# Optimization experiments

Measured on AMD Instinct MI355X. Metric: run time of the kernel, lower is better.

## Reference

```python
import jax, jax.numpy as jnp
import numpy as np

H, W = 4096, 4096

# Fixed tiny kernels expressed as shifted-slice sums (exactly equivalent to
# F.conv2d with stride=1, padding=0 for these 0/1 kernels).

def _diag(x):   # [[1,0],[0,1]] -> (H-1, W-1)
    return x[:-1, :-1] + x[1:, 1:]

def _anti(x):   # [[0,1],[1,0]]
    return x[:-1, 1:] + x[1:, :-1]

def _all2(x):   # 2x2 all-ones
    return x[:-1, :-1] + x[:-1, 1:] + x[1:, :-1] + x[1:, 1:]

def _cross(x):  # 3x3 plus-shape -> (H-2, W-2)
    return x[:-2, 1:-1] + x[2:, 1:-1] + x[1:-1, :-2] + x[1:-1, 2:]

def setup_inputs() -> dict:
    key = jax.random.key(0)
    board = jax.random.randint(key, (H, W), 0, 3, dtype=jnp.int32)
    return {"board_np": board}

def reference(board_np):
    black = (board_np == 1).astype(jnp.float32)
    white = (board_np == 2).astype(jnp.float32)
    empty = (board_np == 0).astype(jnp.float32)

    black_diag, black_anti = _diag(black), _anti(black)
    white_diag, white_anti = _diag(white), _anti(white)
    empty_diag, empty_anti = _diag(empty), _anti(empty)

    bamboo_black = ((black_diag == 2) & (empty_anti == 2)) | ((black_anti == 2) & (empty_diag == 2))
    bamboo_white = ((white_diag == 2) & (empty_anti == 2)) | ((white_anti == 2) & (empty_diag == 2))

    black_s2, white_s2, empty_s2 = _all2(black), _all2(white), _all2(empty)
    # tmp_de/ae/be/ce: single-cell picks of the 2x2 window
    empty_d = empty[1:, 1:]
    empty_a = empty[:-1, :-1]
    empty_b = empty[:-1, 1:]
    empty_c = empty[1:, :-1]
    any_empty_corner = (empty_d == 1) | (empty_a == 1) | (empty_b == 1) | (empty_c == 1)

    tiger_black = (black_s2 >= 2) & any_empty_corner
    tiger_white = (white_s2 >= 2) & any_empty_corner
    empty_triangle_black = (black_s2 == 3) & (empty_s2 == 1)
    empty_triangle_white = (white_s2 == 3) & (empty_s2 == 1)

    empty_center = empty[1:-1, 1:-1]  # k_center conv
    eye_black = (empty_center == 1) & (_cross(black) == 4)
    eye_white = (empty_center == 1) & (_cross(white) == 4)

    return (bamboo_black, bamboo_white, tiger_black, tiger_white,
            empty_triangle_black, empty_triangle_white, eye_black, eye_white)
```

## Files before the change

kernel.cpp:

```cpp
#include <hip/hip_runtime.h>


#define BW 4096
#define W1 4095
#define W2 4094
#define N1 16769025
#define N2 16760836

typedef int i4a __attribute__((vector_size(16), aligned(16)));

template<int IM4>
__device__ __forceinline__ void store_planes(
    int* __restrict__ out, const int i, const int u, const bool has2,
    const int (&cellm)[7], const int (&eyem)[6])
{
    const bool fullv = (u < 1023);
    const size_t orow = (size_t)i * W1 + (u << 2);

    #pragma unroll
    for (int p = 0; p < 6; ++p) {
        const int sp = (IM4 - p) & 3;
        int* dst = out + (size_t)p * N1 + orow;
        if (fullv) {
            i4a s;
            s[0] = (cellm[sp + 0] >> p) & 1;
            s[1] = (cellm[sp + 1] >> p) & 1;
            s[2] = (cellm[sp + 2] >> p) & 1;
            s[3] = (cellm[sp + 3] >> p) & 1;
            *(i4a*)(dst + sp) = s;
        } else {
            #pragma unroll
            for (int k = 0; k < 3 - sp; ++k)
                dst[sp + k] = (cellm[sp + k] >> p) & 1;
        }
        if (u == 0) {
            #pragma unroll
            for (int k = 0; k < sp; ++k)
                dst[k] = (cellm[k] >> p) & 1;
        }
    }

    if (has2) {
        const int e = (IM4 & 1) ? 0 : 2;
        int* d0 = out + (size_t)6 * N1 + (size_t)i * W2 + (u << 2);
        int* d1 = d0 + N2;
        if (fullv) {
            i4a s0, s1;
            #pragma unroll
            for (int k = 0; k < 4; ++k) {
                s0[k] =  eyem[e + k]       & 1;
                s1[k] = (eyem[e + k] >> 1) & 1;
            }
            *(i4a*)(d0 + e) = s0;
            *(i4a*)(d1 + e) = s1;
        } else if (e == 0) {
            #pragma unroll
            for (int k = 0; k < 2; ++k) {
                d0[k] =  eyem[k]       & 1;
                d1[k] = (eyem[k] >> 1) & 1;
            }
        }
        if (u == 0) {
            #pragma unroll
            for (int k = 0; k < e; ++k) {
                d0[k] =  eyem[k]       & 1;
                d1[k] = (eyem[k] >> 1) & 1;
            }
        }
    }
}

__global__ __launch_bounds__(256)
void motif_kernel(const int* __restrict__ board, int* __restrict__ out) {
    const int u = blockIdx.x * 256 + threadIdx.x;
    const int i = blockIdx.y;
    const int base = u << 2;
    const bool fullv = (u < 1023);
    const bool has2  = (i < W2);

    const int* p0 = board + (size_t)i * BW + base;
    const int* p1 = p0 + BW;
    const int* p2 = p1 + BW;

    i4a a0 = *(const i4a*)p0;
    i4a a1 = *(const i4a*)p1;
    i4a b0 = {0, 0, 0, 0}, b1 = {0, 0, 0, 0};
    if (fullv) { b0 = *(const i4a*)(p0 + 4); b1 = *(const i4a*)(p1 + 4); }
    i4a a2 = {0, 0, 0, 0}, b2 = {0, 0, 0, 0};
    if (has2) {
        a2 = *(const i4a*)p2;
        if (fullv) b2 = *(const i4a*)(p2 + 4);
    }

    const int r0[8] = {a0[0], a0[1], a0[2], a0[3], b0[0], b0[1], b0[2], b0[3]};
    const int r1[8] = {a1[0], a1[1], a1[2], a1[3], b1[0], b1[1], b1[2], b1[3]};
    const int r2[8] = {a2[0], a2[1], a2[2], a2[3], b2[0], b2[1], b2[2], b2[3]};

    int cellm[7];
    #pragma unroll
    for (int p = 0; p < 7; ++p) {
        const int a = r0[p], b = r0[p + 1], c = r1[p], d = r1[p + 1];
        const int nb_d = (a == 1) + (d == 1), nb_a = (b == 1) + (c == 1);
        const int nw_d = (a == 2) + (d == 2), nw_a = (b == 2) + (c == 2);
        const int ne_d = (a == 0) + (d == 0), ne_a = (b == 0) + (c == 0);
        const int nb = nb_d + nb_a, nw = nw_d + nw_a, ne = ne_d + ne_a;
        const int bb  = ((nb_d == 2) & (ne_a == 2)) | ((nb_a == 2) & (ne_d == 2));
        const int bw_ = ((nw_d == 2) & (ne_a == 2)) | ((nw_a == 2) & (ne_d == 2));
        const int anyE = (ne >= 1);
        const int tb = (nb >= 2) & anyE;
        const int tw = (nw >= 2) & anyE;
        const int eb = (nb == 3) & (ne == 1);
        const int ew = (nw == 3) & (ne == 1);
        cellm[p] = bb | (bw_ << 1) | (tb << 2) | (tw << 3) | (eb << 4) | (ew << 5);
    }

    int eyem[6];
    #pragma unroll
    for (int q = 0; q < 6; ++q) {
        const int ce = r1[q + 1], up = r0[q + 1], lf = r1[q],
                  dn = r2[q + 1], rt = r1[q + 2];
        const int eB = (ce == 0) & (up == 1) & (lf == 1) & (dn == 1) & (rt == 1);
        const int eW = (ce == 0) & (up == 2) & (lf == 2) & (dn == 2) & (rt == 2);
        eyem[q] = eB | (eW << 1);
    }

    switch (i & 3) {
        case 0: store_planes<0>(out, i, u, has2, cellm, eyem); break;
        case 1: store_planes<1>(out, i, u, has2, cellm, eyem); break;
        case 2: store_planes<2>(out, i, u, has2, cellm, eyem); break;
        case 3: store_planes<3>(out, i, u, has2, cellm, eyem); break;
    }
}

extern "C" void kernel_launch(void* const* d_in, const int* in_sizes, int n_in,
                              void* d_out, int out_size, void* d_ws, size_t ws_size,
                              hipStream_t stream) {
    const int* board = (const int*)d_in[0];
    int* out = (int*)d_out;

    dim3 block(256, 1, 1);
    dim3 grid(4, W1, 1);
    motif_kernel<<<grid, block, 0, stream>>>(board, out);
}
```

Baseline: 599.0 us.

## Process eight rows per thread with a sliding register window of board rows

Each thread now walks eight consecutive output rows. It keeps the previous two board rows in registers and loads only one new row per output row, where before every thread loaded three rows. This cuts redundant global and L2 reads of the board and amortises index setup across rows. In exchange the grid has eight times fewer blocks, which lowers the number of waves available to hide memory latency on the store-heavy output path.

```diff
diff --git a/kernel.cpp b/kernel.cpp
--- a/kernel.cpp
+++ b/kernel.cpp
@@ -6,11 +6,12 @@
 #define W2 4094
 #define N1 16769025
 #define N2 16760836
+#define ROWS 8
 
 typedef int i4a __attribute__((vector_size(16), aligned(16)));
 
-template<int IM4>
-__device__ __forceinline__ void store_planes(
+template<int PH>
+__device__ __forceinline__ void store_row(
     int* __restrict__ out, const int i, const int u, const bool has2,
     const int (&cellm)[7], const int (&eyem)[6])
 {
@@ -19,7 +20,7 @@
 
     #pragma unroll
     for (int p = 0; p < 6; ++p) {
-        const int sp = (IM4 - p) & 3;
+        const int sp = (PH - p) & 3;
         int* dst = out + (size_t)p * N1 + orow;
         if (fullv) {
             i4a s;
@@ -41,7 +42,7 @@
     }
 
     if (has2) {
-        const int e = (IM4 & 1) ? 0 : 2;
+        const int e = (PH & 1) ? 0 : 2;
         int* d0 = out + (size_t)6 * N1 + (size_t)i * W2 + (u << 2);
         int* d1 = d0 + N2;
         if (fullv) {
@@ -72,63 +73,70 @@
 
 __global__ __launch_bounds__(256)
 void motif_kernel(const int* __restrict__ board, int* __restrict__ out) {
-    const int u = blockIdx.x * 256 + threadIdx.x;
-    const int i = blockIdx.y;
+    const int u    = blockIdx.x * 256 + threadIdx.x;
+    const int i0   = blockIdx.y * ROWS;
     const int base = u << 2;
     const bool fullv = (u < 1023);
-    const bool has2  = (i < W2);
 
-    const int* p0 = board + (size_t)i * BW + base;
-    const int* p1 = p0 + BW;
-    const int* p2 = p1 + BW;
+    int r0[8], r1[8], r2[8];
 
-    i4a a0 = *(const i4a*)p0;
-    i4a a1 = *(const i4a*)p1;
-    i4a b0 = {0, 0, 0, 0}, b1 = {0, 0, 0, 0};
-    if (fullv) { b0 = *(const i4a*)(p0 + 4); b1 = *(const i4a*)(p1 + 4); }
-    i4a a2 = {0, 0, 0, 0}, b2 = {0, 0, 0, 0};
-    if (has2) {
-        a2 = *(const i4a*)p2;
-        if (fullv) b2 = *(const i4a*)(p2 + 4);
-    }
+    auto load_row = [&](const int* p, int* w) {
+        i4a v = *(const i4a*)p;
+        w[0] = v[0]; w[1] = v[1]; w[2] = v[2]; w[3] = v[3];
+        if (fullv) {
+            i4a x = *(const i4a*)(p + 4);
+            w[4] = x[0]; w[5] = x[1]; w[6] = x[2]; w[7] = x[3];
+        } else { w[4] = 0; w[5] = 0; w[6] = 0; w[7] = 0; }
+    };
 
-    const int r0[8] = {a0[0], a0[1], a0[2], a0[3], b0[0], b0[1], b0[2], b0[3]};
-    const int r1[8] = {a1[0], a1[1], a1[2], a1[3], b1[0], b1[1], b1[2], b1[3]};
-    const int r2[8] = {a2[0], a2[1], a2[2], a2[3], b2[0], b2[1], b2[2], b2[3]};
+    load_row(board + (size_t)i0 * BW + base, r0);
+    load_row(board + (size_t)(i0 + 1) * BW + base, r1);
 
-    int cellm[7];
     #pragma unroll
-    for (int p = 0; p < 7; ++p) {
-        const int a = r0[p], b = r0[p + 1], c = r1[p], d = r1[p + 1];
-        const int nb_d = (a == 1) + (d == 1), nb_a = (b == 1) + (c == 1);
-        const int nw_d = (a == 2) + (d == 2), nw_a = (b == 2) + (c == 2);
-        const int ne_d = (a == 0) + (d == 0), ne_a = (b == 0) + (c == 0);
-        const int nb = nb_d + nb_a, nw = nw_d + nw_a, ne = ne_d + ne_a;
-        const int bb  = ((nb_d == 2) & (ne_a == 2)) | ((nb_a == 2) & (ne_d == 2));
-        const int bw_ = ((nw_d == 2) & (ne_a == 2)) | ((nw_a == 2) & (ne_d == 2));
-        const int anyE = (ne >= 1);
-        const int tb = (nb >= 2) & anyE;
-        const int tw = (nw >= 2) & anyE;
-        const int eb = (nb == 3) & (ne == 1);
-        const int ew = (nw == 3) & (ne == 1);
-        cellm[p] = bb | (bw_ << 1) | (tb << 2) | (tw << 3) | (eb << 4) | (ew << 5);
-    }
+    for (int r = 0; r < ROWS; ++r) {
+        const int i = i0 + r;
+        if (i >= W1) break;
+        const bool has2 = (i < W2);
+        if (has2)
+            load_row(board + (size_t)(i + 2) * BW + base, r2);
 
-    int eyem[6];
-    #pragma unroll
-    for (int q = 0; q < 6; ++q) {
-        const int ce = r1[q + 1], up = r0[q + 1], lf = r1[q],
-                  dn = r2[q + 1], rt = r1[q + 2];
-        const int eB = (ce == 0) & (up == 1) & (lf == 1) & (dn == 1) & (rt == 1);
-        const int eW = (ce == 0) & (up == 2) & (lf == 2) & (dn == 2) & (rt == 2);
-        eyem[q] = eB | (eW << 1);
-    }
+        int cellm[7];
+        #pragma unroll
+        for (int p = 0; p < 7; ++p) {
+            const int a = r0[p], b = r0[p + 1], c = r1[p], d = r1[p + 1];
+            const int nb_d = (a == 1) + (d == 1), nb_a = (b == 1) + (c == 1);
+            const int nw_d = (a == 2) + (d == 2), nw_a = (b == 2) + (c == 2);
+            const int ne_d = (a == 0) + (d == 0), ne_a = (b == 0) + (c == 0);
+            const int nb = nb_d + nb_a, nw = nw_d + nw_a, ne = ne_d + ne_a;
+            const int bb  = ((nb_d == 2) & (ne_a == 2)) | ((nb_a == 2) & (ne_d == 2));
+            const int bw_ = ((nw_d == 2) & (ne_a == 2)) | ((nw_a == 2) & (ne_d == 2));
+            const int anyE = (ne >= 1);
+            const int tb = (nb >= 2) & anyE;
+            const int tw = (nw >= 2) & anyE;
+            const int eb = (nb == 3) & (ne == 1);
+            const int ew = (nw == 3) & (ne == 1);
+            cellm[p] = bb | (bw_ << 1) | (tb << 2) | (tw << 3) | (eb << 4) | (ew << 5);
+        }
 
-    switch (i & 3) {
-        case 0: store_planes<0>(out, i, u, has2, cellm, eyem); break;
-        case 1: store_planes<1>(out, i, u, has2, cellm, eyem); break;
-        case 2: store_planes<2>(out, i, u, has2, cellm, eyem); break;
-        case 3: store_planes<3>(out, i, u, has2, cellm, eyem); break;
+        int eyem[6];
+        #pragma unroll
+        for (int q = 0; q < 6; ++q) {
+            const int ce = r1[q + 1], up = r0[q + 1], lf = r1[q],
+                      dn = r2[q + 1], rt = r1[q + 2];
+            const int eB = (ce == 0) & (up == 1) & (lf == 1) & (dn == 1) & (rt == 1);
+            const int eW = (ce == 0) & (up == 2) & (lf == 2) & (dn == 2) & (rt == 2);
+            eyem[q] = eB | (eW << 1);
+        }
+
+        switch (r & 3) {
+            case 0: store_row<0>(out, i, u, has2, cellm, eyem); break;
+            case 1: store_row<1>(out, i, u, has2, cellm, eyem); break;
+            case 2: store_row<2>(out, i, u, has2, cellm, eyem); break;
+            case 3: store_row<3>(out, i, u, has2, cellm, eyem); break;
+        }
+
+        #pragma unroll
+        for (int q = 0; q < 8; ++q) { r0[q] = r1[q]; r1[q] = r2[q]; }
     }
 }
 
@@ -139,6 +147,6 @@
     int* out = (int*)d_out;
 
     dim3 block(256, 1, 1);
-    dim3 grid(4, W1, 1);
+    dim3 grid(4, (W1 + ROWS - 1) / ROWS, 1);
     motif_kernel<<<grid, block, 0, stream>>>(board, out);
 }
```

Measured after the change: 614.2 us. 2.5% more time.
